# Performance work log

Hardware: AMD Instinct MI355X
Metric: run time of the kernel (lower is better)

## Reference

```python
import jax, jax.numpy as jnp
import numpy as np

B, SEQ, VOCAB, DIM, DEPTH, HEADS, DH, M, FF, LABELS = 4, 2048, 4096, 768, 6, 12, 64, 256, 3072, 2
INNER = HEADS * DH
EPS_K = 1e-4  # FAVOR+ kernel eps
EPS_LN = 1e-5


def setup_inputs() -> dict:
    key = jax.random.key(0)
    ks = jax.random.split(key, 16)
    g = lambda k, shape: (jax.random.normal(k, shape, jnp.float32) * 0.02)
    return {
        "x": jax.random.randint(ks[0], (B, SEQ), 0, VOCAB),
        "token_emb": g(ks[1], (VOCAB, DIM)),
        "pos_emb": g(ks[2], (SEQ, DIM)),
        "ln1_g": jnp.ones((DEPTH, DIM)), "ln1_b": jnp.zeros((DEPTH, DIM)),
        "Wq": g(ks[3], (DEPTH, DIM, INNER)),
        "Wk": g(ks[4], (DEPTH, DIM, INNER)),
        "Wv": g(ks[5], (DEPTH, DIM, INNER)),
        "Wo": g(ks[6], (DEPTH, INNER, DIM)), "bo": jnp.zeros((DEPTH, DIM)),
        "proj": jax.random.normal(ks[7], (DEPTH, M, DH), jnp.float32),  # FAVOR+ random projections (buffer)
        "ln2_g": jnp.ones((DEPTH, DIM)), "ln2_b": jnp.zeros((DEPTH, DIM)),
        "W1": g(ks[8], (DEPTH, DIM, FF)), "b1": jnp.zeros((DEPTH, FF)),
        "W2": g(ks[9], (DEPTH, FF, DIM)), "b2": jnp.zeros((DEPTH, DIM)),
        "lnf_g": jnp.ones((DIM,)), "lnf_b": jnp.zeros((DIM,)),
        "Wp": g(ks[10], (DIM, DIM)), "bp": jnp.zeros((DIM,)),
        "Wc": g(ks[11], (DIM, LABELS)), "bc": jnp.zeros((LABELS,)),
    }


def layernorm(x, g, b):
    mu = jnp.mean(x, -1, keepdims=True)
    var = jnp.mean(jnp.square(x - mu), -1, keepdims=True)
    return (x - mu) * jax.lax.rsqrt(var + EPS_LN) * g + b


def softmax_kernel(x, proj, is_query):
    # x: [b,h,n,d]  proj: [m,d]   (FAVOR+ positive softmax features)
    d = x.shape[-1]
    m = proj.shape[0]
    dn = d ** -0.25            # data normalizer 1/sqrt(sqrt(d))
    ratio = m ** -0.5
    xd = jnp.einsum('bhnd,md->bhnm', x * dn, proj)
    diag = 0.5 * jnp.sum(jnp.square(x), -1, keepdims=True) * (dn * dn)  # [b,h,n,1]
    if is_query:
        stab = jnp.max(xd, axis=-1, keepdims=True)
    else:
        stab = jnp.max(xd, axis=(-2, -1), keepdims=True)
    return ratio * (jnp.exp(xd - diag - stab) + EPS_K)


def favor_attention(y, Wq, Wk, Wv, Wo, bo, proj):
    b, n, _ = y.shape
    split = lambda t: t.reshape(b, n, HEADS, DH).transpose(0, 2, 1, 3)  # -> bhnd
    q, k, v = split(y @ Wq), split(y @ Wk), split(y @ Wv)
    qp = softmax_kernel(q, proj, True)    # [b,h,n,m]
    kp = softmax_kernel(k, proj, False)   # [b,h,n,m]
    k_sum = jnp.sum(kp, axis=2)                                  # [b,h,m]
    d_inv = 1.0 / jnp.einsum('bhnm,bhm->bhn', qp, k_sum)
    ctx = jnp.einsum('bhnm,bhnd->bhmd', kp, v)                   # [b,h,m,d]
    out = jnp.einsum('bhmd,bhnm,bhn->bhnd', ctx, qp, d_inv)
    out = out.transpose(0, 2, 1, 3).reshape(b, n, INNER)
    return out @ Wo + bo


def reference(x, token_emb, pos_emb, ln1_g, ln1_b, Wq, Wk, Wv, Wo, bo, proj,
              ln2_g, ln2_b, W1, b1, W2, b2, lnf_g, lnf_b, Wp, bp, Wc, bc):
    n = x.shape[1]
    h = token_emb[x] + pos_emb[None, :n]
    for l in range(DEPTH):
        h = h + favor_attention(layernorm(h, ln1_g[l], ln1_b[l]),
                                Wq[l], Wk[l], Wv[l], Wo[l], bo[l], proj[l])
        y = layernorm(h, ln2_g[l], ln2_b[l])
        h = h + (jax.nn.gelu(y @ W1[l] + b1[l], approximate=False) @ W2[l] + b2[l])
    h = layernorm(h, lnf_g, lnf_b)
    pooled = jnp.tanh(h[:, 0] @ Wp + bp)   # BertPooler on first token
    return pooled @ Wc + bc                 # [B, LABELS]
```

## Files before the change

### kernel.cpp

```cpp
#include <hip/hip_runtime.h>
#include <hip/hip_bf16.h>
#include <math.h>

#define B_ 4
#define SEQ_ 2048
#define DIM_ 768
#define DEPTH_ 6
#define HEADS_ 12
#define DH_ 64
#define MF_ 256
#define FF_ 3072
#define ROWS_ 8192
#define BH_ 48
#define QKVW_ 2304
#define DN_ 0.3535533905932738f
#define RATIO_ 0.0625f
#define EPSK_ 1e-4f
#define EPSLN_ 1e-5f

typedef unsigned short u16;
typedef unsigned int   u32;
typedef __bf16 bf16x8 __attribute__((ext_vector_type(8)));
typedef u16    u16x8  __attribute__((ext_vector_type(8)));
typedef float  f32x4  __attribute__((ext_vector_type(4)));

__device__ inline u16 f2bf(float x){
  u32 u = __builtin_bit_cast(u32, x);
  return (u16)((u + 0x7FFFu + ((u>>16)&1u)) >> 16);
}
__device__ inline float bf2f(u16 v){ return __builtin_bit_cast(float, (u32)v<<16); }

__device__ inline void gload16(const u16* g, u16* lds){
  __builtin_amdgcn_global_load_lds(
    (const __attribute__((address_space(1))) u32*)(const void*)g,
    (__attribute__((address_space(3))) u32*)(void*)lds, 16, 0, 0);
}

__global__ void embed_kernel(const int* __restrict__ x, const float4* __restrict__ tok,
                             const float4* __restrict__ pos, float4* __restrict__ h){
  const int C4 = DIM_/4;
  long total = (long)ROWS_*C4;
  for (long i = (long)blockIdx.x*blockDim.x + threadIdx.x; i < total;
       i += (long)gridDim.x*blockDim.x){
    int row = (int)(i / C4); int c = (int)(i - (long)row*C4);
    int n = row & (SEQ_-1);
    float4 a = tok[(long)x[row]*C4 + c];
    float4 p = pos[(long)n*C4 + c];
    float4 o; o.x=a.x+p.x; o.y=a.y+p.y; o.z=a.z+p.z; o.w=a.w+p.w;
    h[i] = o;
  }
}

__global__ __launch_bounds__(256) void ln_kernel(const float* __restrict__ X,
                          const float* __restrict__ g, const float* __restrict__ bta,
                          u16* __restrict__ Y){
  int row = blockIdx.x; int t = threadIdx.x;
  const float* xr = X + (long)row*DIM_;
  float v0 = xr[t], v1 = xr[t+256], v2 = xr[t+512];
  float s = v0+v1+v2;
  float ss = v0*v0+v1*v1+v2*v2;
  int lane = t&63, wid = t>>6;
  #pragma unroll
  for (int off=32; off; off>>=1){ s += __shfl_xor(s,off); ss += __shfl_xor(ss,off); }
  __shared__ float red[8];
  if (lane==0){ red[wid]=s; red[4+wid]=ss; }
  __syncthreads();
  s  = red[0]+red[1]+red[2]+red[3];
  ss = red[4]+red[5]+red[6]+red[7];
  float mu  = s*(1.0f/DIM_);
  float var = ss*(1.0f/DIM_) - mu*mu;
  float rs  = rsqrtf(var + EPSLN_);
  u16* yr = Y + (long)row*DIM_;
  yr[t]     = f2bf((v0-mu)*rs*g[t]     + bta[t]);
  yr[t+256] = f2bf((v1-mu)*rs*g[t+256] + bta[t+256]);
  yr[t+512] = f2bf((v2-mu)*rs*g[t+512] + bta[t+512]);
}

__global__ __launch_bounds__(256) void tconv5_kernel(const float* __restrict__ Wq,
        const float* __restrict__ Wk, const float* __restrict__ Wv,
        const float* __restrict__ Wo, const float* __restrict__ prj,
        u16* __restrict__ dst, u16* __restrict__ phi, u16* __restrict__ plo){
  int z = blockIdx.z;
  if (z == 4){
    int bid = blockIdx.y*24 + blockIdx.x;
    if (bid < 16){
      int i = bid*1024 + threadIdx.x*4;
      float4 v = *(const float4*)(prj + i);
      float vv[4] = {v.x, v.y, v.z, v.w};
      #pragma unroll
      for (int j=0;j<4;j++){
        u16 hh = f2bf(vv[j]);
        phi[i+j] = hh;
        plo[i+j] = f2bf(vv[j] - bf2f(hh));
      }
    }
    return;
  }
  __shared__ float tile[32][33];
  const float* W = (z==0)?Wq:(z==1)?Wk:(z==2)?Wv:Wo;
  u16* WT = dst + (long)z*589824;
  int n0 = blockIdx.x*32, k0 = blockIdx.y*32;
  int tx = threadIdx.x & 31, ty = threadIdx.x >> 5;
  #pragma unroll
  for (int i=0;i<32;i+=8) tile[ty+i][tx] = W[(long)(k0+ty+i)*768 + n0+tx];
  __syncthreads();
  #pragma unroll
  for (int i=0;i<32;i+=8) WT[(long)(n0+ty+i)*768 + k0+tx] = f2bf(tile[tx][ty+i]);
}

__global__ __launch_bounds__(256) void tconvFF_kernel(const float* __restrict__ W1,
        const float* __restrict__ W2, u16* __restrict__ wt1, u16* __restrict__ wt2){
  __shared__ float tile[32][33];
  int z = blockIdx.z;
  const float* W; u16* WT; int K, N, n0, k0;
  if (z==0){ W=W1; WT=wt1; K=768;  N=3072; n0=blockIdx.x*32; k0=blockIdx.y*32; }
  else     { W=W2; WT=wt2; K=3072; N=768;  n0=blockIdx.y*32; k0=blockIdx.x*32; }
  int tx = threadIdx.x & 31, ty = threadIdx.x >> 5;
  #pragma unroll
  for (int i=0;i<32;i+=8) tile[ty+i][tx] = W[(long)(k0+ty+i)*N + n0+tx];
  __syncthreads();
  #pragma unroll
  for (int i=0;i<32;i+=8) WT[(long)(n0+ty+i)*K + k0+tx] = f2bf(tile[tx][ty+i]);
}

template<int FM, int FN, int WM, int WN, int ACT, int CMODE, int BATCH>
__global__ __launch_bounds__(256) void mgemm(const u16* __restrict__ A,
     const u16* __restrict__ BT, const float* __restrict__ bias,
     void* __restrict__ Cv, const float* __restrict__ scale,
     int M, int N, int K, int ldC){
  (void)M;
  constexpr int BM = WM*FM*16, BN = WN*FN*16;
  constexpr int ACH = BM/16, BCH = BN/16;
  __shared__ u16 As[BM*64];
  __shared__ u16 Bs[BN*64];
  int tid = threadIdx.x; int w = tid>>6, l = tid&63;
  int bx, by;
  if (BATCH){ bx = blockIdx.x; by = blockIdx.y; }
  else {
    int bid = blockIdx.y*gridDim.x + blockIdx.x;
    int cpx = (gridDim.x*gridDim.y) >> 3;
    int swz = (bid & 7)*cpx + (bid >> 3);
    bx = swz % gridDim.x; by = swz / gridDim.x;
  }
  int m0 = by*BM, n0 = bx*BN;
  long coff = 0, srow0 = 0;
  if (BATCH){
    int z = blockIdx.z;
    A  += (long)z*2048*K;
    BT += (long)z*(long)N*K;
    coff  = (long)(z/HEADS_)*SEQ_*(long)ldC + (long)(z%HEADS_)*64;
    srow0 = (long)z*SEQ_;
  }
  f32x4 acc[FM][FN];
  #pragma unroll
  for (int i=0;i<FM;i++)
    #pragma unroll
    for (int j=0;j<FN;j++) acc[i][j] = (f32x4){0.f,0.f,0.f,0.f};

  const int row_l = l>>2, cq_l = l&3;
  const int wm = w / WN, wn = w % WN;
  const int kq = l>>4, rl15 = l&15;

  for (int k0=0; k0<K; k0+=64){
    __syncthreads();
    for (int c = w; c < 2*ACH; c += 4){
      int rc = c>>1, ks = c&1;
      int r = rc*16 + row_l;
      int gq = cq_l ^ ((r>>1)&3);
      gload16(A + (long)(m0+r)*K + k0 + ks*32 + gq*8, As + c*512);
    }
    for (int c = w; c < 2*BCH; c += 4){
      int rc = c>>1, ks = c&1;
      int r = rc*16 + row_l;
      int gq = cq_l ^ ((r>>1)&3);
      gload16(BT + (long)(n0+r)*K + k0 + ks*32 + gq*8, Bs + c*512);
    }
    __syncthreads();
    #pragma unroll
    for (int ks=0; ks<2; ks++){
      bf16x8 af[FM], bfr[FN];
      #pragma unroll
      for (int mi=0; mi<FM; mi++){
        int rr = (wm*FM + mi)*16 + rl15;
        int g = kq ^ ((rr>>1)&3);
        af[mi] = *(const bf16x8*)(As + ((rr>>4)*2 + ks)*512 + (rr&15)*32 + g*8);
      }
      #pragma unroll
      for (int ni=0; ni<FN; ni++){
        int rr = (wn*FN + ni)*16 + rl15;
        int g = kq ^ ((rr>>1)&3);
        bfr[ni] = *(const bf16x8*)(Bs + ((rr>>4)*2 + ks)*512 + (rr&15)*32 + g*8);
      }
      #pragma unroll
      for (int mi=0; mi<FM; mi++)
        #pragma unroll
        for (int ni=0; ni<FN; ni++)
          acc[mi][ni] = __builtin_amdgcn_mfma_f32_16x16x32_bf16(af[mi], bfr[ni], acc[mi][ni], 0, 0, 0);
    }
  }

  int cc = l&15, rq = l>>4;
  #pragma unroll
  for (int mi=0; mi<FM; mi++){
    #pragma unroll
    for (int ni=0; ni<FN; ni++){
      int gcol = n0 + (wn*FN+ni)*16 + cc;
      float bv = bias ? bias[gcol] : 0.f;
      #pragma unroll
      for (int r4=0; r4<4; r4++){
        int grow = m0 + (wm*FM+mi)*16 + rq*4 + r4;
        float v = acc[mi][ni][r4] + bv;
        if (ACT) v = 0.5f*v*(1.0f + erff(v*0.70710678118654752f));
        if (CMODE==1){
          float* C = (float*)Cv;
          C[(long)grow*ldC + gcol] += v;
        } else if (CMODE==2){
          v *= scale[srow0 + grow];
          ((u16*)Cv)[coff + (long)grow*ldC + gcol] = f2bf(v);
        } else {
          ((u16*)Cv)[(long)grow*ldC + gcol] = f2bf(v);
        }
      }
    }
  }
}

template<int MODE>
__global__ __launch_bounds__(256) void featgemm(const u16* __restrict__ X,
     const u16* __restrict__ PB, u16* __restrict__ kp,
     float* __restrict__ fmaxbuf, float* __restrict__ ksp){
  __shared__ u16 As[128*32];
  __shared__ u16 Bs[128*32];
  __shared__ float wred[4];
  __shared__ float diag_s[128];
  int tid = threadIdx.x; int w = tid>>6, l = tid&63;
  int n0 = blockIdx.x*128, m0 = blockIdx.y*128;
  int z = blockIdx.z;
  const u16* A = X + (long)(z/HEADS_)*SEQ_*QKVW_ + (z%HEADS_)*DH_;
  float st = 0.f;
  if (MODE==1){
    float mm = (l<32) ? fmaxbuf[z*32 + l] : -1e30f;
    #pragma unroll
    for (int off=32; off; off>>=1) mm = fmaxf(mm, __shfl_xor(mm,off));
    st = mm;
  }
  f32x4 acc[4][4];
  #pragma unroll
  for (int i=0;i<4;i++)
    #pragma unroll
    for (int j=0;j<4;j++) acc[i][j] = (f32x4){0.f,0.f,0.f,0.f};
  float rdiag = 0.f;
  const int row_l = l>>2, cq_l = l&3;
  const int wm = w>>1, wn = w&1;
  const int kq = l>>4, rl15 = l&15;

  for (int k0=0; k0<64; k0+=32){
    __syncthreads();
    for (int c = w; c < 8; c += 4){
      int r = c*16 + row_l;
      int gq = cq_l ^ ((r>>1)&3);
      gload16(A + (long)(m0+r)*QKVW_ + k0 + gq*8, As + c*512);
    }
    for (int c = w; c < 8; c += 4){
      int r = c*16 + row_l;
      int gq = cq_l ^ ((r>>1)&3);
      gload16(PB + (long)(n0+r)*64 + k0 + gq*8, Bs + c*512);
    }
    __syncthreads();
    if (MODE==1){
      int dr = tid>>1, dc = tid&1;
      const u16* rb = As + (dr>>4)*512 + (dr&15)*32 + dc*16;
      u16x8 a0 = *(const u16x8*)rb;
      u16x8 a1 = *(const u16x8*)(rb + 8);
      float s = 0.f;
      #pragma unroll
      for (int j=0;j<8;j++){
        float f0 = bf2f(a0[j]), f1 = bf2f(a1[j]);
        s += f0*f0 + f1*f1;
      }
      s += __shfl_xor(s,1);
      rdiag += s;
    }
    bf16x8 af[4], bfr[4];
    #pragma unroll
    for (int mi=0; mi<4; mi++){
      int rr = (wm*4 + mi)*16 + rl15;
      int g = kq ^ ((rr>>1)&3);
      af[mi] = *(const bf16x8*)(As + rr*32 + g*8);
    }
    #pragma unroll
    for (int ni=0; ni<4; ni++){
      int rr = (wn*4 + ni)*16 + rl15;
      int g = kq ^ ((rr>>1)&3);
      bfr[ni] = *(const bf16x8*)(Bs + rr*32 + g*8);
    }
    #pragma unroll
    for (int mi=0; mi<4; mi++)
      #pragma unroll
      for (int ni=0; ni<4; ni++)
        acc[mi][ni] = __builtin_amdgcn_mfma_f32_16x16x32_bf16(af[mi], bfr[ni], acc[mi][ni], 0, 0, 0);
  }

  if (MODE==0){
    float bm = -1e30f;
    #pragma unroll
    for (int mi=0;mi<4;mi++)
      #pragma unroll
      for (int ni=0;ni<4;ni++)
        #pragma unroll
        for (int r4=0;r4<4;r4++) bm = fmaxf(bm, acc[mi][ni][r4]);
    bm *= DN_;
    #pragma unroll
    for (int off=32; off; off>>=1) bm = fmaxf(bm, __shfl_xor(bm,off));
    if (l==0) wred[w] = bm;
    __syncthreads();
    if (tid==0)
      fmaxbuf[z*32 + blockIdx.y*2 + blockIdx.x] =
        fmaxf(fmaxf(wred[0],wred[1]),fmaxf(wred[2],wred[3]));
  } else {
    if ((tid&1)==0) diag_s[tid>>1] = 0.5f*DN_*DN_*rdiag;
    __syncthreads();
    __shared__ float ksred[128][8];
    int cc = l&15, rq = l>>4;
    #pragma unroll
    for (int ni=0; ni<4; ni++){
      int gcol = n0 + (wn*4+ni)*16 + cc;
      float cs = 0.f;
      #pragma unroll
      for (int mi=0; mi<4; mi++){
        #pragma unroll
        for (int r4=0; r4<4; r4++){
          int lrow = (wm*4+mi)*16 + rq*4 + r4;
          float v = acc[mi][ni][r4]*DN_;
          float e = RATIO_*(expf(v - diag_s[lrow] - st) + EPSK_);
          u16 eb = f2bf(e);
          kp[((long)z*SEQ_ + m0 + lrow)*MF_ + gcol] = eb;
          cs += bf2f(eb);
        }
      }
      ksred[(wn*4+ni)*16 + cc][wm*4 + rq] = cs;
    }
    __syncthreads();
    if (tid < 128){
      float s = 0.f;
      #pragma unroll
      for (int q=0;q<8;q++) s += ksred[tid][q];
      ksp[((long)z*16 + blockIdx.y)*MF_ + n0 + tid] = s;
    }
  }
}

__global__ __launch_bounds__(256) void qfeatgemm(const u16* __restrict__ X,
     const u16* __restrict__ PH, const u16* __restrict__ PL,
     const float* __restrict__ ksp, u16* __restrict__ qp, float* __restrict__ dinv){
  __shared__ u16 As[64*32];
  __shared__ u16 Bh[256*32];
  __shared__ u16 Bl[256*32];
  __shared__ float ksl[256];
  __shared__ float dqs[64];
  __shared__ float rmax[64][4];
  __shared__ float rsum[64][4];
  int tid = threadIdx.x; int w = tid>>6, l = tid&63;
  int n0 = blockIdx.x*64;
  int z = blockIdx.y;
  const u16* A = X + (long)(z/HEADS_)*SEQ_*QKVW_ + (z%HEADS_)*DH_;
  {
    float s = 0.f;
    #pragma unroll
    for (int c=0;c<16;c++) s += ksp[((long)z*16+c)*MF_ + tid];
    ksl[tid] = s;
  }
  f32x4 acc[4][4];
  #pragma unroll
  for (int i=0;i<4;i++)
    #pragma unroll
    for (int j=0;j<4;j++) acc[i][j] = (f32x4){0.f,0.f,0.f,0.f};
  float rdiag = 0.f;
  const int row_l = l>>2, cq_l = l&3;
  const int kq = l>>4, rl15 = l&15;

  for (int k0=0; k0<64; k0+=32){
    __syncthreads();
    {
      int r = w*16 + row_l;
      int gq = cq_l ^ ((r>>1)&3);
      gload16(A + (long)(n0+r)*QKVW_ + k0 + gq*8, As + w*512);
    }
    for (int c = w; c < 16; c += 4){
      int r = c*16 + row_l;
      int gq = cq_l ^ ((r>>1)&3);
      gload16(PH + (long)r*64 + k0 + gq*8, Bh + c*512);
      gload16(PL + (long)r*64 + k0 + gq*8, Bl + c*512);
    }
    __syncthreads();
    {
      int dr = tid>>2, dq4 = tid&3;
      const u16* rb = As + (dr>>4)*512 + (dr&15)*32 + dq4*8;
      u16x8 a0 = *(const u16x8*)rb;
      float s = 0.f;
      #pragma unroll
      for (int j=0;j<8;j++){ float f = bf2f(a0[j]); s += f*f; }
      s += __shfl_xor(s,1); s += __shfl_xor(s,2);
      rdiag += s;
    }
    bf16x8 af[4], bh[4], bl[4];
    #pragma unroll
    for (int mi=0; mi<4; mi++){
      int rr = mi*16 + rl15;
      int g = kq ^ ((rr>>1)&3);
      af[mi] = *(const bf16x8*)(As + rr*32 + g*8);
    }
    #pragma unroll
    for (int ni=0; ni<4; ni++){
      int rr = (w*4 + ni)*16 + rl15;
      int g = kq ^ ((rr>>1)&3);
      bh[ni] = *(const bf16x8*)(Bh + rr*32 + g*8);
      bl[ni] = *(const bf16x8*)(Bl + rr*32 + g*8);
    }
    #pragma unroll
    for (int mi=0; mi<4; mi++)
      #pragma unroll
      for (int ni=0; ni<4; ni++){
        acc[mi][ni] = __builtin_amdgcn_mfma_f32_16x16x32_bf16(af[mi], bh[ni], acc[mi][ni], 0, 0, 0);
        acc[mi][ni] = __builtin_amdgcn_mfma_f32_16x16x32_bf16(af[mi], bl[ni], acc[mi][ni], 0, 0, 0);
      }
  }

  if ((tid&3)==0) dqs[tid>>2] = 0.5f*DN_*DN_*rdiag;
  __syncthreads();

  int cc = l&15, rq = l>>4;
  #pragma unroll
  for (int mi=0; mi<4; mi++){
    #pragma unroll
    for (int r4=0; r4<4; r4++){
      float pm = fmaxf(fmaxf(acc[mi][0][r4],acc[mi][1][r4]),
                       fmaxf(acc[mi][2][r4],acc[mi][3][r4]));
      pm = fmaxf(pm, __shfl_xor(pm,1)); pm = fmaxf(pm, __shfl_xor(pm,2));
      pm = fmaxf(pm, __shfl_xor(pm,4)); pm = fmaxf(pm, __shfl_xor(pm,8));
      if (cc==0) rmax[mi*16 + rq*4 + r4][w] = pm;
    }
  }
  __syncthreads();
  #pragma unroll
  for (int mi=0; mi<4; mi++){
    #pragma unroll
    for (int r4=0; r4<4; r4++){
      int row = mi*16 + rq*4 + r4;
      float mx = fmaxf(fmaxf(rmax[row][0],rmax[row][1]),
                       fmaxf(rmax[row][2],rmax[row][3])) * DN_;
      float dq = dqs[row];
      float dv = 0.f;
      #pragma unroll
      for (int ni=0; ni<4; ni++){
        int col = w*64 + ni*16 + cc;
        float qpv = RATIO_*(expf(acc[mi][ni][r4]*DN_ - dq - mx) + EPSK_);
        u16 qb = f2bf(qpv);
        qp[((long)z*SEQ_ + n0 + row)*MF_ + col] = qb;
        dv += bf2f(qb)*ksl[col];
      }
      dv += __shfl_xor(dv,1); dv += __shfl_xor(dv,2);
      dv += __shfl_xor(dv,4); dv += __shfl_xor(dv,8);
      if (cc==0) rsum[row][w] = dv;
    }
  }
  __syncthreads();
  if (tid < 64){
    float s = rsum[tid][0]+rsum[tid][1]+rsum[tid][2]+rsum[tid][3];
    dinv[(long)z*SEQ_ + n0 + tid] = 1.0f/s;
  }
}

__global__ __launch_bounds__(256) void ctxgemm(const u16* __restrict__ qkv,
     const u16* __restrict__ kp, float* __restrict__ part){
  int kc = blockIdx.x;
  int z  = blockIdx.y;
  int b = z/HEADS_, hh = z%HEADS_;
  int tid = threadIdx.x; int w = tid>>6, l = tid&63;
  __shared__ u16 Vt[64*40];
  __shared__ u16 Kpt[256*40];
  f32x4 acc[4][4];
  #pragma unroll
  for (int i=0;i<4;i++)
    #pragma unroll
    for (int j=0;j<4;j++) acc[i][j] = (f32x4){0.f,0.f,0.f,0.f};
  int n_l = tid&31, grp = tid>>5;
  const int kq = l>>4, rl15 = l&15;
  const long vbase = (long)b*SEQ_*QKVW_ + hh*DH_ + 1536;
  const long kbase = (long)z*SEQ_*MF_;

  for (int s=0; s<32; s++){
    int nG = kc*1024 + s*32 + n_l;
    __syncthreads();
    {
      u16x8 v = *(const u16x8*)(qkv + vbase + (long)nG*QKVW_ + grp*8);
      #pragma unroll
      for (int j=0;j<8;j++) Vt[(grp*8+j)*40 + n_l] = v[j];
    }
    {
      const u16* src = kp + kbase + (long)nG*MF_ + grp*32;
      #pragma unroll
      for (int q=0;q<4;q++){
        u16x8 v = *(const u16x8*)(src + q*8);
        #pragma unroll
        for (int j=0;j<8;j++) Kpt[(grp*32+q*8+j)*40 + n_l] = v[j];
      }
    }
    __syncthreads();
    bf16x8 af[4], bfr[4];
    #pragma unroll
    for (int mi=0; mi<4; mi++)
      af[mi] = *(const bf16x8*)(Vt + (mi*16+rl15)*40 + kq*8);
    #pragma unroll
    for (int ni=0; ni<4; ni++)
      bfr[ni] = *(const bf16x8*)(Kpt + ((w*4+ni)*16+rl15)*40 + kq*8);
    #pragma unroll
    for (int mi=0; mi<4; mi++)
      #pragma unroll
      for (int ni=0; ni<4; ni++)
        acc[mi][ni] = __builtin_amdgcn_mfma_f32_16x16x32_bf16(af[mi], bfr[ni], acc[mi][ni], 0, 0, 0);
  }

  int cc = l&15, rq = l>>4;
  float* pb = part + ((long)kc*BH_ + z)*(64*MF_);
  #pragma unroll
  for (int mi=0; mi<4; mi++){
    #pragma unroll
    for (int ni=0; ni<4; ni++){
      int m = (w*4+ni)*16 + cc;
      #pragma unroll
      for (int r4=0; r4<4; r4++){
        int d = mi*16 + rq*4 + r4;
        pb[(long)d*MF_ + m] = acc[mi][ni][r4];
      }
    }
  }
}

__global__ void ctx_reduce2(const float* __restrict__ part, u16* __restrict__ ctxT){
  const long NT = (long)BH_*64*MF_;
  for (long i = (long)blockIdx.x*256 + threadIdx.x; i < NT; i += (long)gridDim.x*256){
    ctxT[i] = f2bf(part[i] + part[NT + i]);
  }
}

__global__ __launch_bounds__(256) void poolmv_kernel(const float* __restrict__ h,
        const float* __restrict__ g, const float* __restrict__ bta,
        const float* __restrict__ Wp, const float* __restrict__ bp,
        float* __restrict__ pooled){
  int c = blockIdx.x;
  int b = blockIdx.y;
  __shared__ float xs[768];
  __shared__ float red8[8];
  __shared__ float red[64][5];
  int t = threadIdx.x;
  const float* row = h + (long)b*SEQ_*DIM_;
  float v0=row[t], v1=row[t+256], v2=row[t+512];
  float s = v0+v1+v2, ss = v0*v0+v1*v1+v2*v2;
  int lane=t&63, wid=t>>6;
  #pragma unroll
  for (int off=32; off; off>>=1){ s += __shfl_xor(s,off); ss += __shfl_xor(ss,off); }
  if (lane==0){ red8[wid]=s; red8[4+wid]=ss; }
  __syncthreads();
  s  = red8[0]+red8[1]+red8[2]+red8[3];
  ss = red8[4]+red8[5]+red8[6]+red8[7];
  float mu = s*(1.0f/DIM_);
  float var = ss*(1.0f/DIM_) - mu*mu;
  float rs = rsqrtf(var + EPSLN_);
  xs[t]     = (v0-mu)*rs*g[t]     + bta[t];
  xs[t+256] = (v1-mu)*rs*g[t+256] + bta[t+256];
  xs[t+512] = (v2-mu)*rs*g[t+512] + bta[t+512];
  __syncthreads();
  int col_l = t & 63, seg = t >> 6;
  int col = c*64 + col_l;
  const float* wp = Wp + col;
  float a = 0.f;
  #pragma unroll 4
  for (int i = seg*192; i < (seg+1)*192; i++) a += xs[i]*wp[(long)i*DIM_];
  red[col_l][seg] = a;
  __syncthreads();
  if (t < 64){
    float sv = red[t][0]+red[t][1]+red[t][2]+red[t][3] + bp[c*64+t];
    pooled[b*DIM_ + c*64 + t] = tanhf(sv);
  }
}

__global__ __launch_bounds__(256) void cls_kernel(const float* __restrict__ pooled,
        const float* __restrict__ Wc, const float* __restrict__ bc,
        float* __restrict__ out){
  int t = threadIdx.x;
  int b = t >> 6, lane = t & 63;
  float a0 = 0.f, a1 = 0.f;
  for (int i = lane; i < 768; i += 64){
    float p = pooled[b*DIM_ + i];
    a0 += p*Wc[i*2]; a1 += p*Wc[i*2+1];
  }
  #pragma unroll
  for (int off=32; off; off>>=1){ a0 += __shfl_xor(a0,off); a1 += __shfl_xor(a1,off); }
  if (lane==0){ out[b*2] = a0 + bc[0]; out[b*2+1] = a1 + bc[1]; }
}

extern "C" void kernel_launch(void* const* d_in, const int* in_sizes, int n_in,
                              void* d_out, int out_size, void* d_ws, size_t ws_size,
                              hipStream_t stream) {
  (void)in_sizes; (void)n_in; (void)out_size; (void)ws_size;
  const int*   x    = (const int*)  d_in[0];
  const float* tok  = (const float*)d_in[1];
  const float* pos  = (const float*)d_in[2];
  const float* ln1g = (const float*)d_in[3];
  const float* ln1b = (const float*)d_in[4];
  const float* Wq   = (const float*)d_in[5];
  const float* Wk   = (const float*)d_in[6];
  const float* Wv   = (const float*)d_in[7];
  const float* Wo   = (const float*)d_in[8];
  const float* bo   = (const float*)d_in[9];
  const float* proj = (const float*)d_in[10];
  const float* ln2g = (const float*)d_in[11];
  const float* ln2b = (const float*)d_in[12];
  const float* W1   = (const float*)d_in[13];
  const float* b1   = (const float*)d_in[14];
  const float* W2   = (const float*)d_in[15];
  const float* b2   = (const float*)d_in[16];
  const float* lnfg = (const float*)d_in[17];
  const float* lnfb = (const float*)d_in[18];
  const float* Wp   = (const float*)d_in[19];
  const float* bp   = (const float*)d_in[20];
  const float* Wc   = (const float*)d_in[21];
  const float* bc   = (const float*)d_in[22];
  float* out = (float*)d_out;

  char* wsb = (char*)d_ws;
  float* h     = (float*)(wsb + 0);
  u16*   ybf   = (u16*)  (wsb + 25165824);
  float* ctxp2 = (float*)(wsb + 25165824);
  float* ksp   = (float*)(wsb + 32243712);
  float* fmaxp = (float*)(wsb + 33030144);
  float* pooled= (float*)(wsb + 25178112);
  u16*   qkv   = (u16*)  (wsb + 37748736);
  u16*   ffnbf = (u16*)  (wsb + 75497472);
  u16*   kp    = (u16*)  (wsb + 75497472);
  u16*   qp    = (u16*)  (wsb + 75497472);
  u16*   wT    = (u16*)  (wsb + 125829120);
  u16*   ctxT  = (u16*)  (wsb + 139984896);
  float* dinv  = (float*)(wsb + 141557760);
  u16*   projbf= (u16*)  (wsb + 141950976);
  u16*   projlo= (u16*)  (wsb + 141983744);
  u16* attnbf  = ybf;

  u16* wtq = wT;
  u16* wto = wT + 1769472;
  u16* wt1 = wT + 2359296;
  u16* wt2 = wT + 4718592;

  embed_kernel<<<2048,256,0,stream>>>(x,(const float4*)tok,(const float4*)pos,(float4*)h);

  dim3 gD64(6, 128);
  dim3 gQKV(18, 64);
  dim3 gF(24, 64);
  dim3 gQ2(1, 16, BH_);
  dim3 gFG(2, 16, BH_);
  dim3 gQF(32, BH_);

  for (int l=0; l<DEPTH_; l++){
    const float* wq  = Wq + (size_t)l*DIM_*DIM_;
    const float* wk  = Wk + (size_t)l*DIM_*DIM_;
    const float* wv  = Wv + (size_t)l*DIM_*DIM_;
    const float* wo  = Wo + (size_t)l*DIM_*DIM_;
    const float* prj = proj + (size_t)l*MF_*DH_;
    const float* w1  = W1 + (size_t)l*DIM_*FF_;
    const float* w2  = W2 + (size_t)l*FF_*DIM_;

    tconv5_kernel<<<dim3(24,24,5),256,0,stream>>>(wq, wk, wv, wo, prj, wtq, projbf, projlo);
    tconvFF_kernel<<<dim3(96,24,2),256,0,stream>>>(w1, w2, wt1, wt2);

    ln_kernel<<<ROWS_,256,0,stream>>>(h, ln1g+(size_t)l*DIM_, ln1b+(size_t)l*DIM_, ybf);
    mgemm<4,4,2,2,0,0,0><<<gQKV,256,0,stream>>>(ybf, wtq, nullptr, qkv, nullptr, ROWS_, QKVW_, 768, QKVW_);

    featgemm<0><<<gFG,256,0,stream>>>(qkv + 768, projbf, nullptr, fmaxp, nullptr);
    featgemm<1><<<gFG,256,0,stream>>>(qkv + 768, projbf, kp, fmaxp, ksp);
    ctxgemm<<<dim3(2,BH_),256,0,stream>>>(qkv, kp, ctxp2);
    ctx_reduce2<<<768,256,0,stream>>>(ctxp2, ctxT);

    qfeatgemm<<<gQF,256,0,stream>>>(qkv, projbf, projlo, ksp, qp, dinv);
    mgemm<2,4,4,1,0,2,1><<<gQ2,256,0,stream>>>(qp, ctxT, nullptr, attnbf, dinv, SEQ_, 64, 256, 768);

    mgemm<2,4,2,2,0,1,0><<<gD64,256,0,stream>>>(attnbf, wto, bo+(size_t)l*DIM_, h, nullptr, ROWS_, 768, 768, 768);

    ln_kernel<<<ROWS_,256,0,stream>>>(h, ln2g+(size_t)l*DIM_, ln2b+(size_t)l*DIM_, ybf);
    mgemm<4,4,2,2,1,0,0><<<gF,256,0,stream>>>(ybf, wt1, b1+(size_t)l*FF_, ffnbf, nullptr, ROWS_, 3072, 768, 3072);
    mgemm<2,4,2,2,0,1,0><<<gD64,256,0,stream>>>(ffnbf, wt2, b2+(size_t)l*DIM_, h, nullptr, ROWS_, 768, 3072, 768);
  }

  poolmv_kernel<<<dim3(12,B_),256,0,stream>>>(h, lnfg, lnfb, Wp, bp, pooled);
  cls_kernel<<<1,256,0,stream>>>(pooled, Wc, bc, out);
}
```

Before: 2.210 ms.

## Fuse query feature map with context product into one kernel

Merges the query feature kernel and the batched qp×ctx GEMM into a single kernel. The bf16 qp tile and its row normalizer now stay in shared memory (reusing the B staging buffer) instead of being written to and re-read from global memory, and one launch is removed. The ctx operand is read straight from global memory per wave without LDS staging, which may add some redundant loads. The output attention buffer is moved to the region the qp buffer used to occupy.

```diff
diff --git a/kernel.cpp b/kernel.cpp
--- a/kernel.cpp
+++ b/kernel.cpp
@@ -128,7 +128,7 @@
      const u16* __restrict__ BT, const float* __restrict__ bias,
      void* __restrict__ Cv, const float* __restrict__ scale,
      int M, int N, int K, int ldC){
-  (void)M;
+  (void)M; (void)scale;
   constexpr int BM = WM*FM*16, BN = WN*FN*16;
   constexpr int ACH = BM/16, BCH = BN/16;
   __shared__ u16 As[BM*64];
@@ -143,13 +143,10 @@
     bx = swz % gridDim.x; by = swz / gridDim.x;
   }
   int m0 = by*BM, n0 = bx*BN;
-  long coff = 0, srow0 = 0;
   if (BATCH){
     int z = blockIdx.z;
     A  += (long)z*2048*K;
     BT += (long)z*(long)N*K;
-    coff  = (long)(z/HEADS_)*SEQ_*(long)ldC + (long)(z%HEADS_)*64;
-    srow0 = (long)z*SEQ_;
   }
   f32x4 acc[FM][FN];
   #pragma unroll
@@ -214,9 +211,6 @@
         if (CMODE==1){
           float* C = (float*)Cv;
           C[(long)grow*ldC + gcol] += v;
-        } else if (CMODE==2){
-          v *= scale[srow0 + grow];
-          ((u16*)Cv)[coff + (long)grow*ldC + gcol] = f2bf(v);
         } else {
           ((u16*)Cv)[(long)grow*ldC + gcol] = f2bf(v);
         }
@@ -350,20 +344,24 @@
   }
 }
 
-__global__ __launch_bounds__(256) void qfeatgemm(const u16* __restrict__ X,
+__global__ __launch_bounds__(256) void qfeatpv(const u16* __restrict__ X,
      const u16* __restrict__ PH, const u16* __restrict__ PL,
-     const float* __restrict__ ksp, u16* __restrict__ qp, float* __restrict__ dinv){
+     const float* __restrict__ ksp, const u16* __restrict__ ctxT,
+     u16* __restrict__ attn){
   __shared__ u16 As[64*32];
-  __shared__ u16 Bh[256*32];
-  __shared__ u16 Bl[256*32];
+  __shared__ u16 uB[16896];
   __shared__ float ksl[256];
   __shared__ float dqs[64];
   __shared__ float rmax[64][4];
   __shared__ float rsum[64][4];
+  __shared__ float dinvs[64];
+  u16* Bh = uB;
+  u16* Bl = uB + 8192;
   int tid = threadIdx.x; int w = tid>>6, l = tid&63;
   int n0 = blockIdx.x*64;
   int z = blockIdx.y;
-  const u16* A = X + (long)(z/HEADS_)*SEQ_*QKVW_ + (z%HEADS_)*DH_;
+  int b = z/HEADS_, hh = z%HEADS_;
+  const u16* A = X + (long)b*SEQ_*QKVW_ + hh*DH_;
   {
     float s = 0.f;
     #pragma unroll
@@ -456,7 +454,7 @@
         int col = w*64 + ni*16 + cc;
         float qpv = RATIO_*(expf(acc[mi][ni][r4]*DN_ - dq - mx) + EPSK_);
         u16 qb = f2bf(qpv);
-        qp[((long)z*SEQ_ + n0 + row)*MF_ + col] = qb;
+        uB[row*264 + col] = qb;
         dv += bf2f(qb)*ksl[col];
       }
       dv += __shfl_xor(dv,1); dv += __shfl_xor(dv,2);
@@ -467,7 +465,32 @@
   __syncthreads();
   if (tid < 64){
     float s = rsum[tid][0]+rsum[tid][1]+rsum[tid][2]+rsum[tid][3];
-    dinv[(long)z*SEQ_ + n0 + tid] = 1.0f/s;
+    dinvs[tid] = 1.0f/s;
+  }
+  __syncthreads();
+
+  const u16* cz = ctxT + (long)z*(64*MF_);
+  f32x4 acc2[4];
+  #pragma unroll
+  for (int ni=0;ni<4;ni++) acc2[ni] = (f32x4){0.f,0.f,0.f,0.f};
+  #pragma unroll
+  for (int ks2=0; ks2<8; ks2++){
+    bf16x8 aq = *(const bf16x8*)(&uB[(w*16+rl15)*264 + ks2*32 + kq*8]);
+    #pragma unroll
+    for (int ni=0;ni<4;ni++){
+      bf16x8 bv = *(const bf16x8*)(cz + (ni*16+rl15)*MF_ + ks2*32 + kq*8);
+      acc2[ni] = __builtin_amdgcn_mfma_f32_16x16x32_bf16(aq, bv, acc2[ni], 0, 0, 0);
+    }
+  }
+  long cb = ((long)b*SEQ_ + n0)*DIM_ + hh*DH_;
+  #pragma unroll
+  for (int ni=0;ni<4;ni++){
+    #pragma unroll
+    for (int r4=0;r4<4;r4++){
+      int row = w*16 + rq*4 + r4;
+      float v = acc2[ni][r4] * dinvs[row];
+      attn[cb + (long)row*DIM_ + ni*16 + cc] = f2bf(v);
+    }
   }
 }
 
@@ -639,13 +662,11 @@
   u16*   qkv   = (u16*)  (wsb + 37748736);
   u16*   ffnbf = (u16*)  (wsb + 75497472);
   u16*   kp    = (u16*)  (wsb + 75497472);
-  u16*   qp    = (u16*)  (wsb + 75497472);
+  u16*   attnbf= (u16*)  (wsb + 75497472);
   u16*   wT    = (u16*)  (wsb + 125829120);
   u16*   ctxT  = (u16*)  (wsb + 139984896);
-  float* dinv  = (float*)(wsb + 141557760);
   u16*   projbf= (u16*)  (wsb + 141950976);
   u16*   projlo= (u16*)  (wsb + 141983744);
-  u16* attnbf  = ybf;
 
   u16* wtq = wT;
   u16* wto = wT + 1769472;
@@ -657,7 +678,6 @@
   dim3 gD64(6, 128);
   dim3 gQKV(18, 64);
   dim3 gF(24, 64);
-  dim3 gQ2(1, 16, BH_);
   dim3 gFG(2, 16, BH_);
   dim3 gQF(32, BH_);
 
@@ -681,8 +701,7 @@
     ctxgemm<<<dim3(2,BH_),256,0,stream>>>(qkv, kp, ctxp2);
     ctx_reduce2<<<768,256,0,stream>>>(ctxp2, ctxT);
 
-    qfeatgemm<<<gQF,256,0,stream>>>(qkv, projbf, projlo, ksp, qp, dinv);
-    mgemm<2,4,4,1,0,2,1><<<gQ2,256,0,stream>>>(qp, ctxT, nullptr, attnbf, dinv, SEQ_, 64, 256, 768);
+    qfeatpv<<<gQF,256,0,stream>>>(qkv, projbf, projlo, ksp, ctxT, attnbf);
 
     mgemm<2,4,2,2,0,1,0><<<gD64,256,0,stream>>>(attnbf, wto, bo+(size_t)l*DIM_, h, nullptr, ROWS_, 768, 768, 768);
 
```

Measured after the change: 2.228 ms. No clear change (+0.8%).
